# Optimization experiments

Measured on AMD Instinct MI355X. Metric: run time of the kernel, lower is better.

## Reference

```python
import jax, jax.numpy as jnp
import numpy as np

N_NODES, N_EDGES, B, K, D = 200000, 500000, 8192, 32, 128
E_DIM, E_EMB, N_CLASS = 128, 128, 60


def setup_inputs() -> dict:
    key = jax.random.key(0)
    ks = jax.random.split(key, 16)
    s = lambda k, shape, scale=0.05: jax.random.normal(k, shape, dtype=jnp.float32) * scale
    return {
        'memory_emb': s(ks[0], (N_NODES, D), 1.0),
        'edge_feat': s(ks[1], (N_EDGES, E_DIM), 1.0),
        'W_q': s(ks[2], (D, D)),
        'W_k': s(ks[3], (D, D)),
        'a': s(ks[4], (2 * D,)),
        'We_w': s(ks[5], (E_DIM, E_EMB)),
        'We_b': s(ks[6], (E_EMB,)),
        'Wuc': s(ks[7], (D + 2 * D + E_EMB, D)),
        'Wc1': s(ks[8], (D, 128)),
        'Wc2': s(ks[9], (128, N_CLASS)),
        'src_idxs': jax.random.randint(ks[10], (B,), 0, N_NODES),
        'dst_idxs': jax.random.randint(ks[11], (B,), 0, N_NODES),
        'edge_idxs': jax.random.randint(ks[12], (B,), 0, N_EDGES),
        'src_neighbors': jax.random.randint(ks[13], (B, K), 0, N_NODES),
        'dst_neighbors': jax.random.randint(ks[14], (B, K), 0, N_NODES),
    }


def reference(memory_emb, edge_feat, W_q, W_k, a, We_w, We_b, Wuc, Wc1, Wc2,
              src_idxs, dst_idxs, edge_idxs, src_neighbors, dst_neighbors):
    def attend(idxs, nbrs):
        self_emb = memory_emb[idxs]                      # [B, D] gather
        nb = memory_emb[nbrs]                            # [B, K, D] gather
        q = self_emb @ W_q                               # [B, D]
        k = jnp.einsum('bkd,de->bke', nb, W_k)           # [B, K, D]
        # GAT-style score: leaky_relu(a . [q || k])
        sq = q @ a[:D]                                   # [B]
        sk = jnp.einsum('bkd,d->bk', k, a[D:])           # [B, K]
        score = jax.nn.leaky_relu(sq[:, None] + sk, 0.2)
        attn = jax.nn.softmax(score, axis=-1)            # [B, K]
        agg = jnp.einsum('bk,bkd->bd', attn, k)          # [B, D]
        return self_emb, agg

    src_e, src_h = attend(src_idxs, src_neighbors)
    dst_e, dst_h = attend(dst_idxs, dst_neighbors)
    e = edge_feat[edge_idxs] @ We_w + We_b               # edge embedding [B, E_EMB]
    msg_src = jax.nn.relu(jnp.concatenate([src_e, src_h, dst_h, e], -1) @ Wuc)
    msg_dst = jax.nn.relu(jnp.concatenate([dst_e, dst_h, src_h, e], -1) @ Wuc)
    logits_src = jax.nn.relu(msg_src @ Wc1) @ Wc2
    logits_dst = jax.nn.relu(msg_dst @ Wc1) @ Wc2
    return jnp.stack([logits_src, logits_dst])           # [2, B, N_CLASS]
```

## Files before the change

### kernel.cpp

```cpp
#include <hip/hip_runtime.h>

#define D 128
#define KNBR 32
#define BATCH 8192
#define NCLASS 60
#define NB 16
#define NP 32

__device__ __forceinline__ unsigned short f2bf_rne(float f) {
    unsigned int x = __float_as_uint(f);
    x = x + 0x7FFFu + ((x >> 16) & 1u);
    return (unsigned short)(x >> 16);
}

__global__ __launch_bounds__(256) void k_prep(
    const float* __restrict__ Wq, const float* __restrict__ Wk,
    const float* __restrict__ a, const float* __restrict__ Wew,
    const float* __restrict__ Web, const float* __restrict__ Wuc,
    float* __restrict__ wqa, float* __restrict__ wka,
    float* __restrict__ be, float* __restrict__ Wcomb2)
{
    __shared__ float sB[128][129];
    int blk = blockIdx.x, tid = threadIdx.x;
    if (blk == 0) {
        for (int t = tid; t < 128 * 128; t += 256) sB[t >> 7][t & 127] = Wq[t];
        __syncthreads();
        if (tid < 128) {
            float s = 0.f;
            for (int j = 0; j < D; ++j) s += sB[tid][j] * a[j];
            wqa[tid] = s;
        }
        __syncthreads();
        for (int t = tid; t < 128 * 128; t += 256) sB[t >> 7][t & 127] = Wk[t];
        __syncthreads();
        if (tid < 128) {
            float s = 0.f;
            for (int j = 0; j < D; ++j) s += sB[tid][j] * a[D + j];
            wka[tid] = s;
        }
    } else if (blk == 1) {
        if (tid < 128) {
            float acc = 0.f;
            for (int j = 0; j < D; ++j) acc += Web[j] * Wuc[(size_t)(384 + j) * D + tid];
            be[tid] = acc;
        }
    } else {
        int g  = (blk - 2) >> 4;
        int rb = ((blk - 2) & 15) * 8;
        const float* A = (g == 2) ? Wew : Wk;
        const float* B = Wuc + (size_t)(128 + g * 128) * D;
        for (int t = tid; t < 128 * 128; t += 256) sB[t >> 7][t & 127] = B[t];
        __syncthreads();
        int j = tid & 127, half = tid >> 7;
        float acc[4] = {0.f, 0.f, 0.f, 0.f};
        int r0 = rb + half * 4;
        for (int t = 0; t < 128; ++t) {
            float bv = sB[t][j];
            #pragma unroll
            for (int m = 0; m < 4; ++m)
                acc[m] = fmaf(A[(size_t)(r0 + m) * D + t], bv, acc[m]);
        }
        #pragma unroll
        for (int m = 0; m < 4; ++m)
            Wcomb2[(size_t)(g * 128 + r0 + m) * D + j] = acc[m];
    }
}

__global__ __launch_bounds__(256) void k_scores(
    const float* __restrict__ mem,
    const float* __restrict__ wqa, const float* __restrict__ wka,
    float* __restrict__ nsq, float* __restrict__ nsk,
    unsigned short* __restrict__ memh)
{
    int tid = threadIdx.x, lane = tid & 31, grp = tid >> 5;
    int n0 = blockIdx.x * 64 + grp * 8;
    float4 wq4 = ((const float4*)wqa)[lane];
    float4 wk4 = ((const float4*)wka)[lane];
    #pragma unroll
    for (int i = 0; i < 8; ++i) {
        int n = n0 + i;
        float4 v = ((const float4*)(mem + (size_t)n * D))[lane];
        ushort4 hv;
        hv.x = f2bf_rne(v.x); hv.y = f2bf_rne(v.y);
        hv.z = f2bf_rne(v.z); hv.w = f2bf_rne(v.w);
        ((ushort4*)(memh + (size_t)n * D))[lane] = hv;

        float pq = v.x * wq4.x + v.y * wq4.y + v.z * wq4.z + v.w * wq4.w;
        float pk = v.x * wk4.x + v.y * wk4.y + v.z * wk4.z + v.w * wk4.w;
        #pragma unroll
        for (int m = 1; m <= 16; m <<= 1) {
            pq += __shfl_xor(pq, m, 32);
            pk += __shfl_xor(pk, m, 32);
        }
        if (lane == 0) nsq[n] = pq;
        if (lane == 1) nsk[n] = pk;
    }
}

__global__ __launch_bounds__(256) void k_attn(
    const unsigned short* __restrict__ memh,
    const float* __restrict__ nsq, const float* __restrict__ nsk,
    const int* __restrict__ src_idxs, const int* __restrict__ dst_idxs,
    const int* __restrict__ src_nb, const int* __restrict__ dst_nb,
    float* __restrict__ agg)
{
    int lane = threadIdx.x & 63;
    int wid  = threadIdx.x >> 6;
    int p    = blockIdx.x * 4 + wid;
    int side = p >> 13;
    int b    = p & (BATCH - 1);

    int self_idx = (side ? dst_idxs : src_idxs)[b];
    int ik = (side ? dst_nb : src_nb)[(size_t)b * KNBR + (lane & 31)];

    float x = nsq[self_idx] + nsk[ik];
    x = (x >= 0.f) ? x : 0.2f * x;
    float mx = x;
    #pragma unroll
    for (int m = 1; m <= 16; m <<= 1) mx = fmaxf(mx, __shfl_xor(mx, m, 32));
    float e = __expf(x - mx);
    float s = e;
    #pragma unroll
    for (int m = 1; m <= 16; m <<= 1) s += __shfl_xor(s, m, 32);
    float attn = e / s;

    int rsub = lane >> 4;
    int lr   = lane & 15;

    float acc[8];
    #pragma unroll
    for (int j = 0; j < 8; ++j) acc[j] = 0.f;

    #pragma unroll
    for (int k0 = 0; k0 < KNBR; k0 += 4) {
        int   k   = k0 + rsub;
        int   ikk = __shfl(ik, k, 64);
        float ak  = __shfl(attn, k, 64);
        uint4 hv = *(const uint4*)(memh + (size_t)ikk * D + lr * 8);
        acc[0] = fmaf(ak, __uint_as_float(hv.x << 16),          acc[0]);
        acc[1] = fmaf(ak, __uint_as_float(hv.x & 0xFFFF0000u),  acc[1]);
        acc[2] = fmaf(ak, __uint_as_float(hv.y << 16),          acc[2]);
        acc[3] = fmaf(ak, __uint_as_float(hv.y & 0xFFFF0000u),  acc[3]);
        acc[4] = fmaf(ak, __uint_as_float(hv.z << 16),          acc[4]);
        acc[5] = fmaf(ak, __uint_as_float(hv.z & 0xFFFF0000u),  acc[5]);
        acc[6] = fmaf(ak, __uint_as_float(hv.w << 16),          acc[6]);
        acc[7] = fmaf(ak, __uint_as_float(hv.w & 0xFFFF0000u),  acc[7]);
    }
    #pragma unroll
    for (int j = 0; j < 8; ++j) {
        acc[j] += __shfl_xor(acc[j], 16, 64);
        acc[j] += __shfl_xor(acc[j], 32, 64);
    }
    float* orow = agg + (size_t)p * D + lr * 8;
    if (rsub == 0) *(float4*)orow       = make_float4(acc[0], acc[1], acc[2], acc[3]);
    if (rsub == 1) *(float4*)(orow + 4) = make_float4(acc[4], acc[5], acc[6], acc[7]);
}

__global__ __launch_bounds__(256, 3) void k_gemm(
    const float* __restrict__ mem, const float* __restrict__ edge_feat,
    const float* __restrict__ Wuc, const float* __restrict__ Wcomb2,
    const float* __restrict__ be, const float* __restrict__ agg,
    const float* __restrict__ Wc1, const float* __restrict__ Wc2,
    const int* __restrict__ src_idxs, const int* __restrict__ dst_idxs,
    const int* __restrict__ edge_idxs,
    float* __restrict__ out)
{
    __shared__ __align__(16) float Ws[32 * 128];
    __shared__ __align__(16) float nbT[128 * 33];
    __shared__ __align__(16) float uni[128 * 33];
    __shared__ int s_sidx[NP];
    __shared__ int s_eidx[NB];

    int tid = threadIdx.x;
    int b0 = blockIdx.x * NB;
    int lane = tid & 31;
    int grp  = tid >> 5;

    if (tid < NP) s_sidx[tid] = ((tid >> 4) ? dst_idxs : src_idxs)[b0 + (tid & 15)];
    if (tid < NB) s_eidx[tid] = edge_idxs[b0 + tid];

    #pragma unroll
    for (int q = 0; q < 4; ++q) {
        int pp = grp + 8 * q;
        int gp = ((pp >> 4) ? BATCH : 0) + b0 + (pp & 15);
        float4 v = ((const float4*)(agg + (size_t)gp * D))[lane];
        nbT[(lane * 4 + 0) * 33 + pp] = v.x;
        nbT[(lane * 4 + 1) * 33 + pp] = v.y;
        nbT[(lane * 4 + 2) * 33 + pp] = v.z;
        nbT[(lane * 4 + 3) * 33 + pp] = v.w;
    }
    __syncthreads();

    int tr = tid >> 4, tc = tid & 15;
    int lc = tid & 31, lr = tid >> 5;
    int wc = tid & 127, wk2 = tid >> 7;
    float accB[2][8];
    #pragma unroll
    for (int i = 0; i < 2; ++i)
        #pragma unroll
        for (int j = 0; j < 8; ++j) accB[i][j] = 0.f;

    float* Ast = uni;

    for (int kt = 0; kt < 4; ++kt) {
        int off = kt * 32;
        #pragma unroll
        for (int q = 0; q < 4; ++q) {
            int r = lr + 8 * q;
            Ast[lc * 33 + r] = mem[(size_t)s_sidx[r] * D + off + lc];
        }
        #pragma unroll
        for (int pp = 0; pp < 16; ++pp) {
            int kk = wk2 + 2 * pp;
            Ws[kk * 128 + wc] = Wuc[(size_t)(off + kk) * D + wc];
        }
        __syncthreads();
        #pragma unroll 8
        for (int kk = 0; kk < 32; ++kk) {
            float a0 = Ast[kk * 33 + tr * 2];
            float a1 = Ast[kk * 33 + tr * 2 + 1];
            float4 w0 = *(const float4*)&Ws[kk * 128 + tc * 4];
            float4 w1 = *(const float4*)&Ws[kk * 128 + 64 + tc * 4];
            float wr[8] = {w0.x, w0.y, w0.z, w0.w, w1.x, w1.y, w1.z, w1.w};
            #pragma unroll
            for (int j = 0; j < 8; ++j) {
                accB[0][j] = fmaf(a0, wr[j], accB[0][j]);
                accB[1][j] = fmaf(a1, wr[j], accB[1][j]);
            }
        }
        __syncthreads();
    }
    for (int kt = 4; kt < 12; ++kt) {
        int off = (kt & 3) * 32;
        int gr0 = kt * 32 - 128;
        #pragma unroll
        for (int pp = 0; pp < 16; ++pp) {
            int kk = wk2 + 2 * pp;
            Ws[kk * 128 + wc] = Wcomb2[(size_t)(gr0 + kk) * D + wc];
        }
        __syncthreads();
        int r0 = (kt < 8) ? (tr * 2) : ((tr * 2) ^ 16);
        #pragma unroll 8
        for (int kk = 0; kk < 32; ++kk) {
            float a0 = nbT[(off + kk) * 33 + r0];
            float a1 = nbT[(off + kk) * 33 + r0 + 1];
            float4 w0 = *(const float4*)&Ws[kk * 128 + tc * 4];
            float4 w1 = *(const float4*)&Ws[kk * 128 + 64 + tc * 4];
            float wr[8] = {w0.x, w0.y, w0.z, w0.w, w1.x, w1.y, w1.z, w1.w};
            #pragma unroll
            for (int j = 0; j < 8; ++j) {
                accB[0][j] = fmaf(a0, wr[j], accB[0][j]);
                accB[1][j] = fmaf(a1, wr[j], accB[1][j]);
            }
        }
        __syncthreads();
    }
    for (int kt = 12; kt < 16; ++kt) {
        int off = (kt & 3) * 32;
        int gr0 = kt * 32 - 128;
        #pragma unroll
        for (int q = 0; q < 4; ++q) {
            int r = lr + 8 * q;
            Ast[lc * 33 + r] = edge_feat[(size_t)s_eidx[r & 15] * D + off + lc];
        }
        #pragma unroll
        for (int pp = 0; pp < 16; ++pp) {
            int kk = wk2 + 2 * pp;
            Ws[kk * 128 + wc] = Wcomb2[(size_t)(gr0 + kk) * D + wc];
        }
        __syncthreads();
        #pragma unroll 8
        for (int kk = 0; kk < 32; ++kk) {
            float a0 = Ast[kk * 33 + tr * 2];
            float a1 = Ast[kk * 33 + tr * 2 + 1];
            float4 w0 = *(const float4*)&Ws[kk * 128 + tc * 4];
            float4 w1 = *(const float4*)&Ws[kk * 128 + 64 + tc * 4];
            float wr[8] = {w0.x, w0.y, w0.z, w0.w, w1.x, w1.y, w1.z, w1.w};
            #pragma unroll
            for (int j = 0; j < 8; ++j) {
                accB[0][j] = fmaf(a0, wr[j], accB[0][j]);
                accB[1][j] = fmaf(a1, wr[j], accB[1][j]);
            }
        }
        __syncthreads();
    }

    float* msgT = uni;
    {
        float4 bv0 = *(const float4*)&be[tc * 4];
        float4 bv1 = *(const float4*)&be[64 + tc * 4];
        float b8[8] = {bv0.x, bv0.y, bv0.z, bv0.w, bv1.x, bv1.y, bv1.z, bv1.w};
        #pragma unroll
        for (int i = 0; i < 2; ++i) {
            int r = tr * 2 + i;
            #pragma unroll
            for (int j = 0; j < 4; ++j) {
                msgT[(tc * 4 + j) * 33 + r]      = fmaxf(accB[i][j] + b8[j], 0.f);
                msgT[(64 + tc * 4 + j) * 33 + r] = fmaxf(accB[i][j + 4] + b8[j + 4], 0.f);
            }
        }
    }
    __syncthreads();

    float accC[2][8];
    #pragma unroll
    for (int i = 0; i < 2; ++i)
        #pragma unroll
        for (int j = 0; j < 8; ++j) accC[i][j] = 0.f;

    for (int kt = 0; kt < 4; ++kt) {
        int off = kt * 32;
        #pragma unroll
        for (int pp = 0; pp < 16; ++pp) {
            int kk = wk2 + 2 * pp;
            Ws[kk * 128 + wc] = Wc1[(size_t)(off + kk) * D + wc];
        }
        __syncthreads();
        #pragma unroll 8
        for (int kk = 0; kk < 32; ++kk) {
            float a0 = msgT[(off + kk) * 33 + tr * 2];
            float a1 = msgT[(off + kk) * 33 + tr * 2 + 1];
            float4 w0 = *(const float4*)&Ws[kk * 128 + tc * 4];
            float4 w1 = *(const float4*)&Ws[kk * 128 + 64 + tc * 4];
            float wr[8] = {w0.x, w0.y, w0.z, w0.w, w1.x, w1.y, w1.z, w1.w};
            #pragma unroll
            for (int j = 0; j < 8; ++j) {
                accC[0][j] = fmaf(a0, wr[j], accC[0][j]);
                accC[1][j] = fmaf(a1, wr[j], accC[1][j]);
            }
        }
        __syncthreads();
    }
    #pragma unroll
    for (int i = 0; i < 2; ++i) {
        int r = tr * 2 + i;
        #pragma unroll
        for (int j = 0; j < 4; ++j) {
            msgT[(tc * 4 + j) * 33 + r]      = fmaxf(accC[i][j], 0.f);
            msgT[(64 + tc * 4 + j) * 33 + r] = fmaxf(accC[i][j + 4], 0.f);
        }
    }
    __syncthreads();

    int r2 = tid & 31;
    int cs = tid >> 5;
    float acc2[8];
    #pragma unroll
    for (int j = 0; j < 8; ++j) acc2[j] = 0.f;

    for (int kt = 0; kt < 4; ++kt) {
        int off = kt * 32;
        for (int t = tid; t < 32 * 64; t += 256) {
            int kk = t >> 6, c = t & 63;
            Ws[t] = (c < NCLASS) ? Wc2[(size_t)(off + kk) * NCLASS + c] : 0.f;
        }
        __syncthreads();
        #pragma unroll 4
        for (int kk = 0; kk < 32; ++kk) {
            float h = msgT[(off + kk) * 33 + r2];
            float4 w0 = *(const float4*)&Ws[kk * 64 + cs * 8];
            float4 w1 = *(const float4*)&Ws[kk * 64 + cs * 8 + 4];
            acc2[0] = fmaf(h, w0.x, acc2[0]);
            acc2[1] = fmaf(h, w0.y, acc2[1]);
            acc2[2] = fmaf(h, w0.z, acc2[2]);
            acc2[3] = fmaf(h, w0.w, acc2[3]);
            acc2[4] = fmaf(h, w1.x, acc2[4]);
            acc2[5] = fmaf(h, w1.y, acc2[5]);
            acc2[6] = fmaf(h, w1.z, acc2[6]);
            acc2[7] = fmaf(h, w1.w, acc2[7]);
        }
        __syncthreads();
    }
    {
        int side = r2 >> 4;
        int bb = b0 + (r2 & 15);
        size_t orow = ((size_t)side * BATCH + bb) * NCLASS;
        #pragma unroll
        for (int j = 0; j < 8; ++j) {
            int c = cs * 8 + j;
            if (c < NCLASS) out[orow + c] = acc2[j];
        }
    }
}

extern "C" void kernel_launch(void* const* d_in, const int* in_sizes, int n_in,
                              void* d_out, int out_size, void* d_ws, size_t ws_size,
                              hipStream_t stream) {
    const float* mem       = (const float*)d_in[0];
    const float* edge_feat = (const float*)d_in[1];
    const float* Wq        = (const float*)d_in[2];
    const float* Wk        = (const float*)d_in[3];
    const float* a         = (const float*)d_in[4];
    const float* Wew       = (const float*)d_in[5];
    const float* Web       = (const float*)d_in[6];
    const float* Wuc       = (const float*)d_in[7];
    const float* Wc1       = (const float*)d_in[8];
    const float* Wc2       = (const float*)d_in[9];
    const int* src_idxs    = (const int*)d_in[10];
    const int* dst_idxs    = (const int*)d_in[11];
    const int* edge_idxs   = (const int*)d_in[12];
    const int* src_nb      = (const int*)d_in[13];
    const int* dst_nb      = (const int*)d_in[14];
    float* out = (float*)d_out;

    float* ws = (float*)d_ws;
    float* Wcomb2 = ws;
    float* be     = ws + 49152;
    float* wqa    = ws + 49280;
    float* wka    = ws + 49408;
    float* nsq    = ws + 49536;
    float* nsk    = ws + 249536;
    float* agg    = ws + 449536;
    unsigned short* memh = (unsigned short*)(ws + 2546688);

    k_prep<<<50, 256, 0, stream>>>(Wq, Wk, a, Wew, Web, Wuc, wqa, wka, be, Wcomb2);
    k_scores<<<200000 / 64, 256, 0, stream>>>(mem, wqa, wka, nsq, nsk, memh);
    k_attn<<<2 * BATCH / 4, 256, 0, stream>>>(memh, nsq, nsk, src_idxs, dst_idxs,
                                              src_nb, dst_nb, agg);
    k_gemm<<<BATCH / NB, 256, 0, stream>>>(mem, edge_feat, Wuc, Wcomb2, be, agg,
                                           Wc1, Wc2,
                                           src_idxs, dst_idxs, edge_idxs, out);
}
```

Measured before the change: 492.0 us.

## Store agg in bf16 and stage full bf16 A operand in shared memory

The attention kernel now writes its aggregated output as bf16 instead of fp32, which halves that intermediate's traffic. The gemm kernel gathers the self embedding (from the bf16 memory copy), both aggregates and the edge features into one bf16 shared tile before the K loop. The three separate K-loop phases become a single 16-step loop that streams only weights. This removes per-tile gathers and syncs, but adds bf16 rounding of agg and edge features, and the larger shared footprint lowers launch bounds from 3 to 2 blocks per CU.

```diff
diff --git a/kernel.cpp b/kernel.cpp
--- a/kernel.cpp
+++ b/kernel.cpp
@@ -102,7 +102,7 @@
     const float* __restrict__ nsq, const float* __restrict__ nsk,
     const int* __restrict__ src_idxs, const int* __restrict__ dst_idxs,
     const int* __restrict__ src_nb, const int* __restrict__ dst_nb,
-    float* __restrict__ agg)
+    unsigned short* __restrict__ aggh)
 {
     int lane = threadIdx.x & 63;
     int wid  = threadIdx.x >> 6;
@@ -151,48 +151,78 @@
         acc[j] += __shfl_xor(acc[j], 16, 64);
         acc[j] += __shfl_xor(acc[j], 32, 64);
     }
-    float* orow = agg + (size_t)p * D + lr * 8;
-    if (rsub == 0) *(float4*)orow       = make_float4(acc[0], acc[1], acc[2], acc[3]);
-    if (rsub == 1) *(float4*)(orow + 4) = make_float4(acc[4], acc[5], acc[6], acc[7]);
-}
-
-__global__ __launch_bounds__(256, 3) void k_gemm(
-    const float* __restrict__ mem, const float* __restrict__ edge_feat,
+    if (rsub == 0) {
+        ushort4 hv;
+        hv.x = f2bf_rne(acc[0]); hv.y = f2bf_rne(acc[1]);
+        hv.z = f2bf_rne(acc[2]); hv.w = f2bf_rne(acc[3]);
+        *(ushort4*)(aggh + (size_t)p * D + lr * 8) = hv;
+    } else if (rsub == 1) {
+        ushort4 hv;
+        hv.x = f2bf_rne(acc[4]); hv.y = f2bf_rne(acc[5]);
+        hv.z = f2bf_rne(acc[6]); hv.w = f2bf_rne(acc[7]);
+        *(ushort4*)(aggh + (size_t)p * D + lr * 8 + 4) = hv;
+    }
+}
+
+__global__ __launch_bounds__(256, 2) void k_gemm(
+    const unsigned short* __restrict__ memh, const float* __restrict__ edge_feat,
     const float* __restrict__ Wuc, const float* __restrict__ Wcomb2,
-    const float* __restrict__ be, const float* __restrict__ agg,
+    const float* __restrict__ be, const unsigned short* __restrict__ aggh,
     const float* __restrict__ Wc1, const float* __restrict__ Wc2,
     const int* __restrict__ src_idxs, const int* __restrict__ dst_idxs,
     const int* __restrict__ edge_idxs,
     float* __restrict__ out)
 {
+    __shared__ __align__(16) unsigned short Afull[512 * 34];
     __shared__ __align__(16) float Ws[32 * 128];
-    __shared__ __align__(16) float nbT[128 * 33];
-    __shared__ __align__(16) float uni[128 * 33];
-    __shared__ int s_sidx[NP];
-    __shared__ int s_eidx[NB];
 
     int tid = threadIdx.x;
     int b0 = blockIdx.x * NB;
-    int lane = tid & 31;
-    int grp  = tid >> 5;
-
-    if (tid < NP) s_sidx[tid] = ((tid >> 4) ? dst_idxs : src_idxs)[b0 + (tid & 15)];
-    if (tid < NB) s_eidx[tid] = edge_idxs[b0 + tid];
-
-    #pragma unroll
-    for (int q = 0; q < 4; ++q) {
-        int pp = grp + 8 * q;
-        int gp = ((pp >> 4) ? BATCH : 0) + b0 + (pp & 15);
-        float4 v = ((const float4*)(agg + (size_t)gp * D))[lane];
-        nbT[(lane * 4 + 0) * 33 + pp] = v.x;
-        nbT[(lane * 4 + 1) * 33 + pp] = v.y;
-        nbT[(lane * 4 + 2) * 33 + pp] = v.z;
-        nbT[(lane * 4 + 3) * 33 + pp] = v.w;
+
+    for (int t = tid; t < 512; t += 256) {
+        int p = t >> 4, c0 = (t & 15) * 8;
+        int sidx = ((p >> 4) ? dst_idxs : src_idxs)[b0 + (p & 15)];
+        uint4 v = *(const uint4*)(memh + (size_t)sidx * D + c0);
+        const unsigned short* us = (const unsigned short*)&v;
+        #pragma unroll
+        for (int j = 0; j < 8; ++j) Afull[(c0 + j) * 34 + p] = us[j];
+    }
+    for (int t = tid; t < 512; t += 256) {
+        int p = t >> 4, c0 = (t & 15) * 8;
+        int gp = ((p >> 4) ? BATCH : 0) + b0 + (p & 15);
+        uint4 v = *(const uint4*)(aggh + (size_t)gp * D + c0);
+        const unsigned short* us = (const unsigned short*)&v;
+        #pragma unroll
+        for (int j = 0; j < 8; ++j) Afull[(128 + c0 + j) * 34 + p] = us[j];
+    }
+    for (int t = tid; t < 512; t += 256) {
+        int p = t >> 4, c0 = (t & 15) * 8;
+        int gp = ((p >> 4) ? 0 : BATCH) + b0 + (p & 15);
+        uint4 v = *(const uint4*)(aggh + (size_t)gp * D + c0);
+        const unsigned short* us = (const unsigned short*)&v;
+        #pragma unroll
+        for (int j = 0; j < 8; ++j) Afull[(256 + c0 + j) * 34 + p] = us[j];
+    }
+    {
+        int e = tid >> 4, c0 = (tid & 15) * 8;
+        int eidx = edge_idxs[b0 + e];
+        const float* src = edge_feat + (size_t)eidx * D + c0;
+        float4 v0 = *(const float4*)src;
+        float4 v1 = *(const float4*)(src + 4);
+        unsigned short us[8];
+        us[0] = f2bf_rne(v0.x); us[1] = f2bf_rne(v0.y);
+        us[2] = f2bf_rne(v0.z); us[3] = f2bf_rne(v0.w);
+        us[4] = f2bf_rne(v1.x); us[5] = f2bf_rne(v1.y);
+        us[6] = f2bf_rne(v1.z); us[7] = f2bf_rne(v1.w);
+        #pragma unroll
+        for (int j = 0; j < 8; ++j) {
+            Afull[(384 + c0 + j) * 34 + e]      = us[j];
+            Afull[(384 + c0 + j) * 34 + e + 16] = us[j];
+        }
     }
     __syncthreads();
 
     int tr = tid >> 4, tc = tid & 15;
-    int lc = tid & 31, lr = tid >> 5;
     int wc = tid & 127, wk2 = tid >> 7;
     float accB[2][8];
     #pragma unroll
@@ -200,25 +230,21 @@
         #pragma unroll
         for (int j = 0; j < 8; ++j) accB[i][j] = 0.f;
 
-    float* Ast = uni;
-
-    for (int kt = 0; kt < 4; ++kt) {
-        int off = kt * 32;
-        #pragma unroll
-        for (int q = 0; q < 4; ++q) {
-            int r = lr + 8 * q;
-            Ast[lc * 33 + r] = mem[(size_t)s_sidx[r] * D + off + lc];
-        }
+    for (int kt = 0; kt < 16; ++kt) {
+        const float* Wsrc = (kt < 4) ? (Wuc + (size_t)(kt * 32) * D)
+                                     : (Wcomb2 + (size_t)(kt * 32 - 128) * D);
         #pragma unroll
         for (int pp = 0; pp < 16; ++pp) {
             int kk = wk2 + 2 * pp;
-            Ws[kk * 128 + wc] = Wuc[(size_t)(off + kk) * D + wc];
-        }
-        __syncthreads();
+            Ws[kk * 128 + wc] = Wsrc[(size_t)kk * D + wc];
+        }
+        __syncthreads();
+        const unsigned short* Acol = Afull + (size_t)(kt * 32) * 34 + 2 * tr;
         #pragma unroll 8
         for (int kk = 0; kk < 32; ++kk) {
-            float a0 = Ast[kk * 33 + tr * 2];
-            float a1 = Ast[kk * 33 + tr * 2 + 1];
+            unsigned int av = *(const unsigned int*)(Acol + kk * 34);
+            float a0 = __uint_as_float(av << 16);
+            float a1 = __uint_as_float(av & 0xFFFF0000u);
             float4 w0 = *(const float4*)&Ws[kk * 128 + tc * 4];
             float4 w1 = *(const float4*)&Ws[kk * 128 + 64 + tc * 4];
             float wr[8] = {w0.x, w0.y, w0.z, w0.w, w1.x, w1.y, w1.z, w1.w};
@@ -230,62 +256,8 @@
         }
         __syncthreads();
     }
-    for (int kt = 4; kt < 12; ++kt) {
-        int off = (kt & 3) * 32;
-        int gr0 = kt * 32 - 128;
-        #pragma unroll
-        for (int pp = 0; pp < 16; ++pp) {
-            int kk = wk2 + 2 * pp;
-            Ws[kk * 128 + wc] = Wcomb2[(size_t)(gr0 + kk) * D + wc];
-        }
-        __syncthreads();
-        int r0 = (kt < 8) ? (tr * 2) : ((tr * 2) ^ 16);
-        #pragma unroll 8
-        for (int kk = 0; kk < 32; ++kk) {
-            float a0 = nbT[(off + kk) * 33 + r0];
-            float a1 = nbT[(off + kk) * 33 + r0 + 1];
-            float4 w0 = *(const float4*)&Ws[kk * 128 + tc * 4];
-            float4 w1 = *(const float4*)&Ws[kk * 128 + 64 + tc * 4];
-            float wr[8] = {w0.x, w0.y, w0.z, w0.w, w1.x, w1.y, w1.z, w1.w};
-            #pragma unroll
-            for (int j = 0; j < 8; ++j) {
-                accB[0][j] = fmaf(a0, wr[j], accB[0][j]);
-                accB[1][j] = fmaf(a1, wr[j], accB[1][j]);
-            }
-        }
-        __syncthreads();
-    }
-    for (int kt = 12; kt < 16; ++kt) {
-        int off = (kt & 3) * 32;
-        int gr0 = kt * 32 - 128;
-        #pragma unroll
-        for (int q = 0; q < 4; ++q) {
-            int r = lr + 8 * q;
-            Ast[lc * 33 + r] = edge_feat[(size_t)s_eidx[r & 15] * D + off + lc];
-        }
-        #pragma unroll
-        for (int pp = 0; pp < 16; ++pp) {
-            int kk = wk2 + 2 * pp;
-            Ws[kk * 128 + wc] = Wcomb2[(size_t)(gr0 + kk) * D + wc];
-        }
-        __syncthreads();
-        #pragma unroll 8
-        for (int kk = 0; kk < 32; ++kk) {
-            float a0 = Ast[kk * 33 + tr * 2];
-            float a1 = Ast[kk * 33 + tr * 2 + 1];
-            float4 w0 = *(const float4*)&Ws[kk * 128 + tc * 4];
-            float4 w1 = *(const float4*)&Ws[kk * 128 + 64 + tc * 4];
-            float wr[8] = {w0.x, w0.y, w0.z, w0.w, w1.x, w1.y, w1.z, w1.w};
-            #pragma unroll
-            for (int j = 0; j < 8; ++j) {
-                accB[0][j] = fmaf(a0, wr[j], accB[0][j]);
-                accB[1][j] = fmaf(a1, wr[j], accB[1][j]);
-            }
-        }
-        __syncthreads();
-    }
-
-    float* msgT = uni;
+
+    float* msgT = (float*)Afull;
     {
         float4 bv0 = *(const float4*)&be[tc * 4];
         float4 bv1 = *(const float4*)&be[64 + tc * 4];
@@ -410,14 +382,14 @@
     float* wka    = ws + 49408;
     float* nsq    = ws + 49536;
     float* nsk    = ws + 249536;
-    float* agg    = ws + 449536;
+    unsigned short* aggh = (unsigned short*)(ws + 449536);
     unsigned short* memh = (unsigned short*)(ws + 2546688);
 
     k_prep<<<50, 256, 0, stream>>>(Wq, Wk, a, Wew, Web, Wuc, wqa, wka, be, Wcomb2);
     k_scores<<<200000 / 64, 256, 0, stream>>>(mem, wqa, wka, nsq, nsk, memh);
     k_attn<<<2 * BATCH / 4, 256, 0, stream>>>(memh, nsq, nsk, src_idxs, dst_idxs,
-                                              src_nb, dst_nb, agg);
-    k_gemm<<<BATCH / NB, 256, 0, stream>>>(mem, edge_feat, Wuc, Wcomb2, be, agg,
+                                              src_nb, dst_nb, aggh);
+    k_gemm<<<BATCH / NB, 256, 0, stream>>>(memh, edge_feat, Wuc, Wcomb2, be, aggh,
                                            Wc1, Wc2,
                                            src_idxs, dst_idxs, edge_idxs, out);
 }
```

After: 478.9 us. 1.03x faster.
